# Performance work log

Hardware: AMD Instinct MI355X
Metric: run time of the kernel (lower is better)

## Reference

```python
import jax, jax.numpy as jnp
import numpy as np

K = 7  # kernel_size


def _patches(x, k):
    # x: [N, C, H, W] -> [K*K, N, C, H, W]; zero-padded local windows in
    # torch.nn.functional.unfold order (kernel positions row-major).
    N, C, H, W = x.shape
    p = k // 2
    xp = jnp.pad(x, ((0, 0), (0, 0), (p, p), (p, p)))
    return jnp.stack([xp[:, :, i:i + H, j:j + W]
                      for i in range(k) for j in range(k)], axis=0)


def setup_inputs() -> dict:
    key = jax.random.key(0)
    k1, k2 = jax.random.split(key)
    x = jax.random.normal(k1, (4, 128, 80, 80), dtype=jnp.float32)
    feat_in = jax.random.normal(k2, (4, 128, 80, 80), dtype=jnp.float32)
    return {"x": x, "feat_in": feat_in}


def reference(x, feat_in):
    N, C, H, W = feat_in.shape
    k2 = K * K
    # theta_x == phi_x == x in the original module.
    phi_p = _patches(x, K)                            # [K2, N, Cq, H, W]
    # local dot products: weight[k, n, h, w] = sum_c phi_window * theta_center
    w = jnp.einsum('knchw,nchw->knhw', phi_p, x)      # [K2, N, H, W]
    # L1-style normalization over the window (plain sum, as in the source)
    w = w / jnp.sum(w, axis=0, keepdims=True)
    feat_p = _patches(feat_in, K)                     # [K2, N, C, H, W]
    out = jnp.einsum('knhw,knchw->nchw', w, feat_p)   # [N, C, H, W]
    pairwise_weight = w.transpose(1, 2, 3, 0).reshape(N * H * W, 1, k2)
    return out, pairwise_weight
```

## Files before the change

### kernel.cpp

```cpp
#include <hip/hip_runtime.h>


namespace {

constexpr int CN = 4;
constexpr int CC = 128;
constexpr int HT = 80, WD = 80;
constexpr int KK = 7, K2 = 49, PD = 3;
constexpr int TW = 16, TH = 4;
constexpr int HW_ = TW + 6;
constexpr int HH_ = TH + 6;
constexpr int HENT = HW_ * HH_;
constexpr int HFLT = HENT * 4;
constexpr int HCHUNK = (HFLT + 63) / 64;
constexpr int HPADF = HCHUNK * 64;
constexpr int PLANE = HT * WD;
constexpr int GSTRIDE = 4 * PLANE;
constexpr int OUT_ELEMS = CN * CC * PLANE;

__device__ __forceinline__ void issue_chunks(const float* gbase, const int* off,
                                             float* lds, int tid) {
#if __has_builtin(__builtin_amdgcn_global_load_lds)
#pragma unroll
  for (int q = 0; q < HCHUNK; ++q) {
    __builtin_amdgcn_global_load_lds(
        (const __attribute__((address_space(1))) void*)(gbase + off[q]),
        (__attribute__((address_space(3))) void*)(lds + q * 64), 4, 0, 0);
  }
#else
#pragma unroll
  for (int q = 0; q < HCHUNK; ++q) lds[q * 64 + tid] = gbase[off[q]];
  asm volatile("s_waitcnt lgkmcnt(0)" ::: "memory");
#endif
}

#define WAIT_VM(n_lit)                                      \
  asm volatile("s_waitcnt vmcnt(" #n_lit ")" ::: "memory"); \
  __builtin_amdgcn_sched_barrier(0)

__global__ __launch_bounds__(64) void lnl2d_fused(const float* __restrict__ x,
                                                  const float* __restrict__ feat,
                                                  float* __restrict__ dout) {
  __shared__ float halo[2][HPADF];
  __shared__ float wstage[TH * TW * K2];

  const int tid = (int)threadIdx.x;
  const int tx = tid & (TW - 1);
  const int ty = tid >> 4;
  const int bx = (int)blockIdx.x;
  const int by = (int)blockIdx.y;
  const int n  = (int)blockIdx.z;

  const int h = by * TH + ty;
  const int w = bx * TW + tx;

  const float* xn = x + (size_t)n * CC * PLANE;
  const float* fn = feat + (size_t)n * CC * PLANE;
  float* out = dout;
  float* pw  = dout + OUT_ELEMS;

  int off[HCHUNK];
#pragma unroll
  for (int q = 0; q < HCHUNK; ++q) {
    int f = q * 64 + tid;
    int e = f >> 2;
    if (e > HENT - 1) e = HENT - 1;
    const int ch = f & 3;
    const int r  = e / HW_;
    const int cl = e - r * HW_;
    int gh = by * TH - PD + r;
    gh = gh < 0 ? 0 : (gh > HT - 1 ? HT - 1 : gh);
    int gw = bx * TW - PD + cl;
    gw = gw < 0 ? 0 : (gw > WD - 1 ? WD - 1 : gw);
    off[q] = ch * PLANE + gh * WD + gw;
  }

  float acc[K2];
#pragma unroll
  for (int k = 0; k < K2; ++k) acc[k] = 0.f;

  auto p1_compute = [&](const float* hb) {
    const float4 c4 = *(const float4*)(hb + ((ty + PD) * HW_ + (tx + PD)) * 4);
#pragma unroll
    for (int di = 0; di < KK; ++di) {
#pragma unroll
      for (int dj = 0; dj < KK; ++dj) {
        const float4 n4 = *(const float4*)(hb + ((ty + di) * HW_ + (tx + dj)) * 4);
        acc[di * KK + dj] += c4.x * n4.x + c4.y * n4.y + c4.z * n4.z + c4.w * n4.w;
      }
    }
  };

  issue_chunks(xn, off, halo[0], tid);
  int goff = GSTRIDE;
  for (int g = 0; g < 31; ++g) {
    issue_chunks(xn + goff, off, halo[(g + 1) & 1], tid);
    goff += GSTRIDE;
    WAIT_VM(14);
    p1_compute(halo[g & 1]);
  }
  issue_chunks(fn, off, halo[0], tid);
  WAIT_VM(14);
  p1_compute(halo[1]);

#pragma unroll
  for (int di = 0; di < KK; ++di) {
#pragma unroll
    for (int dj = 0; dj < KK; ++dj) {
      const int hh = h + di - PD, ww = w + dj - PD;
      if ((unsigned)hh >= (unsigned)HT || (unsigned)ww >= (unsigned)WD)
        acc[di * KK + dj] = 0.f;
    }
  }
  float ssum = 0.f;
#pragma unroll
  for (int k = 0; k < K2; ++k) ssum += acc[k];
  const float invs = 1.0f / ssum;
#pragma unroll
  for (int k = 0; k < K2; ++k) acc[k] *= invs;

#pragma unroll
  for (int k = 0; k < K2; ++k) wstage[tid * K2 + k] = acc[k];
  __syncthreads();
#pragma unroll
  for (int r = 0; r < TH; ++r) {
    float* dst = pw + (size_t)(n * PLANE + (by * TH + r) * WD + bx * TW) * K2;
    const float* src = wstage + r * TW * K2;
#pragma unroll
    for (int c2 = 0; c2 < (TW * K2) / 64; ++c2)
      dst[c2 * 64 + tid] = src[c2 * 64 + tid];
    if (tid < (TW * K2) - 64 * ((TW * K2) / 64))
      dst[64 * ((TW * K2) / 64) + tid] = src[64 * ((TW * K2) / 64) + tid];
  }

  const size_t obase = (size_t)n * CC * PLANE + (size_t)(h * WD + w);
  auto p2_compute = [&](const float* hb, int g) {
    float4 a = make_float4(0.f, 0.f, 0.f, 0.f);
#pragma unroll
    for (int di = 0; di < KK; ++di) {
#pragma unroll
      for (int dj = 0; dj < KK; ++dj) {
        const float4 n4 = *(const float4*)(hb + ((ty + di) * HW_ + (tx + dj)) * 4);
        const float wk = acc[di * KK + dj];
        a.x += wk * n4.x; a.y += wk * n4.y; a.z += wk * n4.z; a.w += wk * n4.w;
      }
    }
    out[obase + (size_t)(4 * g + 0) * PLANE] = a.x;
    out[obase + (size_t)(4 * g + 1) * PLANE] = a.y;
    out[obase + (size_t)(4 * g + 2) * PLANE] = a.z;
    out[obase + (size_t)(4 * g + 3) * PLANE] = a.w;
  };

  goff = GSTRIDE;
  for (int g = 0; g < 31; ++g) {
    issue_chunks(fn + goff, off, halo[(g + 1) & 1], tid);
    goff += GSTRIDE;
    WAIT_VM(14);
    p2_compute(halo[g & 1], g);
  }
  WAIT_VM(0);
  p2_compute(halo[1], 31);
}

}

extern "C" void kernel_launch(void* const* d_in, const int* in_sizes, int n_in,
                              void* d_out, int out_size, void* d_ws, size_t ws_size,
                              hipStream_t stream) {
  const float* x    = (const float*)d_in[0];
  const float* feat = (const float*)d_in[1];
  float* out        = (float*)d_out;
  dim3 grid(WD / TW, HT / TH, CN);
  lnl2d_fused<<<grid, 64, 0, stream>>>(x, feat, out);
}
```

Baseline: 170.1 us.

## Split fused kernel into channel-chunked correlation and aggregation kernels via workspace

```diff
diff --git a/kernel.cpp b/kernel.cpp
--- a/kernel.cpp
+++ b/kernel.cpp
@@ -3,63 +3,23 @@
 
 namespace {
 
-constexpr int CN = 4;
-constexpr int CC = 128;
-constexpr int HT = 80, WD = 80;
+constexpr int CN = 4, CC = 128, HT = 80, WD = 80;
 constexpr int KK = 7, K2 = 49, PD = 3;
 constexpr int TW = 16, TH = 4;
 constexpr int HW_ = TW + 6;
 constexpr int HH_ = TH + 6;
 constexpr int HENT = HW_ * HH_;
-constexpr int HFLT = HENT * 4;
-constexpr int HCHUNK = (HFLT + 63) / 64;
+constexpr int HCHUNK = (HENT * 4 + 63) / 64;
 constexpr int HPADF = HCHUNK * 64;
 constexpr int PLANE = HT * WD;
 constexpr int GSTRIDE = 4 * PLANE;
 constexpr int OUT_ELEMS = CN * CC * PLANE;
-
-__device__ __forceinline__ void issue_chunks(const float* gbase, const int* off,
-                                             float* lds, int tid) {
-#if __has_builtin(__builtin_amdgcn_global_load_lds)
-#pragma unroll
-  for (int q = 0; q < HCHUNK; ++q) {
-    __builtin_amdgcn_global_load_lds(
-        (const __attribute__((address_space(1))) void*)(gbase + off[q]),
-        (__attribute__((address_space(3))) void*)(lds + q * 64), 4, 0, 0);
-  }
-#else
-#pragma unroll
-  for (int q = 0; q < HCHUNK; ++q) lds[q * 64 + tid] = gbase[off[q]];
-  asm volatile("s_waitcnt lgkmcnt(0)" ::: "memory");
-#endif
-}
-
-#define WAIT_VM(n_lit)                                      \
-  asm volatile("s_waitcnt vmcnt(" #n_lit ")" ::: "memory"); \
-  __builtin_amdgcn_sched_barrier(0)
-
-__global__ __launch_bounds__(64) void lnl2d_fused(const float* __restrict__ x,
-                                                  const float* __restrict__ feat,
-                                                  float* __restrict__ dout) {
-  __shared__ float halo[2][HPADF];
-  __shared__ float wstage[TH * TW * K2];
-
-  const int tid = (int)threadIdx.x;
-  const int tx = tid & (TW - 1);
-  const int ty = tid >> 4;
-  const int bx = (int)blockIdx.x;
-  const int by = (int)blockIdx.y;
-  const int n  = (int)blockIdx.z;
-
-  const int h = by * TH + ty;
-  const int w = bx * TW + tx;
-
-  const float* xn = x + (size_t)n * CC * PLANE;
-  const float* fn = feat + (size_t)n * CC * PLANE;
-  float* out = dout;
-  float* pw  = dout + OUT_ELEMS;
-
-  int off[HCHUNK];
+constexpr int CHUNKS = 4, GPC = 8;
+constexpr int NTILES = 5 * 20 * CN;
+constexpr int WPAD = 52;
+constexpr size_t WS_NEED = (size_t)CHUNKS * NTILES * 64 * WPAD * 4;
+
+__device__ __forceinline__ void make_off(int* off, int bx, int by, int tid) {
 #pragma unroll
   for (int q = 0; q < HCHUNK; ++q) {
     int f = q * 64 + tid;
@@ -74,21 +34,218 @@
     gw = gw < 0 ? 0 : (gw > WD - 1 ? WD - 1 : gw);
     off[q] = ch * PLANE + gh * WD + gw;
   }
+}
+
+__device__ __forceinline__ void issue_chunks(const float* gbase, const int* off,
+                                             float* lds, int tid) {
+#if __has_builtin(__builtin_amdgcn_global_load_lds)
+#pragma unroll
+  for (int q = 0; q < HCHUNK; ++q) {
+    __builtin_amdgcn_global_load_lds(
+        (const __attribute__((address_space(1))) void*)(gbase + off[q]),
+        (__attribute__((address_space(3))) void*)(lds + q * 64), 4, 0, 0);
+  }
+#else
+#pragma unroll
+  for (int q = 0; q < HCHUNK; ++q) lds[q * 64 + tid] = gbase[off[q]];
+  asm volatile("s_waitcnt lgkmcnt(0)" ::: "memory");
+#endif
+}
+
+#define WAIT_VM(n_lit)                                      \
+  asm volatile("s_waitcnt vmcnt(" #n_lit ")" ::: "memory"); \
+  __builtin_amdgcn_sched_barrier(0)
+
+__global__ __launch_bounds__(64) void lnl2d_corr(const float* __restrict__ x,
+                                                 float* __restrict__ wpart) {
+  __shared__ float halo[3][HPADF];
+  __shared__ float wstage[64 * WPAD];
+
+  const int tid = (int)threadIdx.x;
+  const int tx = tid & (TW - 1), ty = tid >> 4;
+  const int bx = (int)blockIdx.x, by = (int)blockIdx.y;
+  const int z = (int)blockIdx.z, n = z >> 2, chunk = z & 3;
+  const int tile = (n * 20 + by) * 5 + bx;
+
+  const float* xc = x + (size_t)n * CC * PLANE + (size_t)chunk * 32 * PLANE;
+
+  int off[HCHUNK];
+  make_off(off, bx, by, tid);
 
   float acc[K2];
 #pragma unroll
   for (int k = 0; k < K2; ++k) acc[k] = 0.f;
 
-  auto p1_compute = [&](const float* hb) {
+  issue_chunks(xc, off, halo[0], tid);
+  issue_chunks(xc + GSTRIDE, off, halo[1], tid);
+  int goff = 2 * GSTRIDE;
+#pragma unroll
+  for (int g = 0; g < GPC; ++g) {
+    if (g < GPC - 2) { issue_chunks(xc + goff, off, halo[(g + 2) % 3], tid); goff += GSTRIDE; }
+    if (g < GPC - 2)      { WAIT_VM(28); }
+    else if (g == GPC - 2){ WAIT_VM(14); }
+    else                  { WAIT_VM(0); }
+    const float* hb = halo[g % 3];
     const float4 c4 = *(const float4*)(hb + ((ty + PD) * HW_ + (tx + PD)) * 4);
 #pragma unroll
-    for (int di = 0; di < KK; ++di) {
+    for (int di = 0; di < KK; ++di)
 #pragma unroll
       for (int dj = 0; dj < KK; ++dj) {
         const float4 n4 = *(const float4*)(hb + ((ty + di) * HW_ + (tx + dj)) * 4);
         acc[di * KK + dj] += c4.x * n4.x + c4.y * n4.y + c4.z * n4.z + c4.w * n4.w;
       }
+  }
+
+  const int h = by * TH + ty, w = bx * TW + tx;
+#pragma unroll
+  for (int di = 0; di < KK; ++di)
+#pragma unroll
+    for (int dj = 0; dj < KK; ++dj) {
+      const int hh = h + di - PD, ww = w + dj - PD;
+      if ((unsigned)hh >= (unsigned)HT || (unsigned)ww >= (unsigned)WD)
+        acc[di * KK + dj] = 0.f;
     }
+
+#pragma unroll
+  for (int k = 0; k < K2; ++k) wstage[tid * WPAD + k] = acc[k];
+#pragma unroll
+  for (int k = K2; k < WPAD; ++k) wstage[tid * WPAD + k] = 0.f;
+  __syncthreads();
+  float4* dst = (float4*)(wpart + ((size_t)(chunk * NTILES + tile) * 64) * WPAD);
+  const float4* src = (const float4*)wstage;
+#pragma unroll
+  for (int i = 0; i < (64 * WPAD) / 4 / 64; ++i)
+    dst[i * 64 + tid] = src[i * 64 + tid];
+}
+
+__global__ __launch_bounds__(64) void lnl2d_agg(const float* __restrict__ feat,
+                                                const float* __restrict__ wpart,
+                                                float* __restrict__ dout) {
+  __shared__ float halo[3][HPADF];
+  __shared__ float wstage[64 * WPAD];
+
+  const int tid = (int)threadIdx.x;
+  const int tx = tid & (TW - 1), ty = tid >> 4;
+  const int bx = (int)blockIdx.x, by = (int)blockIdx.y;
+  const int z = (int)blockIdx.z, n = z >> 2, chunk = z & 3;
+  const int tile = (n * 20 + by) * 5 + bx;
+  const int h = by * TH + ty, w = bx * TW + tx;
+
+  const float* fc = feat + (size_t)n * CC * PLANE + (size_t)chunk * 32 * PLANE;
+  float* out = dout;
+  float* pw  = dout + OUT_ELEMS;
+
+  int off[HCHUNK];
+  make_off(off, bx, by, tid);
+
+  float4 wv[WPAD / 4];
+#pragma unroll
+  for (int i = 0; i < WPAD / 4; ++i) wv[i] = make_float4(0.f, 0.f, 0.f, 0.f);
+#pragma unroll
+  for (int c = 0; c < CHUNKS; ++c) {
+    const float4* p =
+        (const float4*)(wpart + ((size_t)(c * NTILES + tile) * 64 + tid) * WPAD);
+#pragma unroll
+    for (int i = 0; i < WPAD / 4; ++i) {
+      const float4 v = p[i];
+      wv[i].x += v.x; wv[i].y += v.y; wv[i].z += v.z; wv[i].w += v.w;
+    }
+  }
+  float wk[K2];
+#pragma unroll
+  for (int k = 0; k < K2; ++k) wk[k] = ((const float*)wv)[k];
+  float ssum = 0.f;
+#pragma unroll
+  for (int k = 0; k < K2; ++k) ssum += wk[k];
+  const float invs = 1.0f / ssum;
+#pragma unroll
+  for (int k = 0; k < K2; ++k) wk[k] *= invs;
+
+  WAIT_VM(0);
+
+  float4 ov[GPC];
+#pragma unroll
+  for (int g = 0; g < GPC; ++g) ov[g] = make_float4(0.f, 0.f, 0.f, 0.f);
+
+  issue_chunks(fc, off, halo[0], tid);
+  issue_chunks(fc + GSTRIDE, off, halo[1], tid);
+  int goff = 2 * GSTRIDE;
+#pragma unroll
+  for (int g = 0; g < GPC; ++g) {
+    if (g < GPC - 2) { issue_chunks(fc + goff, off, halo[(g + 2) % 3], tid); goff += GSTRIDE; }
+    if (g < GPC - 2)      { WAIT_VM(28); }
+    else if (g == GPC - 2){ WAIT_VM(14); }
+    else                  { WAIT_VM(0); }
+    const float* hb = halo[g % 3];
+#pragma unroll
+    for (int di = 0; di < KK; ++di)
+#pragma unroll
+      for (int dj = 0; dj < KK; ++dj) {
+        const float4 n4 = *(const float4*)(hb + ((ty + di) * HW_ + (tx + dj)) * 4);
+        const float f = wk[di * KK + dj];
+        ov[g].x += f * n4.x; ov[g].y += f * n4.y; ov[g].z += f * n4.z; ov[g].w += f * n4.w;
+      }
+  }
+
+  const size_t ob = (size_t)n * CC * PLANE + (size_t)chunk * 32 * PLANE +
+                    (size_t)(h * WD + w);
+#pragma unroll
+  for (int g = 0; g < GPC; ++g) {
+    out[ob + (size_t)(4 * g + 0) * PLANE] = ov[g].x;
+    out[ob + (size_t)(4 * g + 1) * PLANE] = ov[g].y;
+    out[ob + (size_t)(4 * g + 2) * PLANE] = ov[g].z;
+    out[ob + (size_t)(4 * g + 3) * PLANE] = ov[g].w;
+  }
+
+  if (chunk == 0) {
+#pragma unroll
+    for (int k = 0; k < K2; ++k) wstage[tid * K2 + k] = wk[k];
+    __syncthreads();
+#pragma unroll
+    for (int r = 0; r < TH; ++r) {
+      float* dst = pw + (size_t)(n * PLANE + (by * TH + r) * WD + bx * TW) * K2;
+      const float* src = wstage + r * TW * K2;
+#pragma unroll
+      for (int c2 = 0; c2 < (TW * K2) / 64; ++c2)
+        dst[c2 * 64 + tid] = src[c2 * 64 + tid];
+      if (tid < (TW * K2) - 64 * ((TW * K2) / 64))
+        dst[64 * ((TW * K2) / 64) + tid] = src[64 * ((TW * K2) / 64) + tid];
+    }
+  }
+}
+
+__global__ __launch_bounds__(64) void lnl2d_fused(const float* __restrict__ x,
+                                                  const float* __restrict__ feat,
+                                                  float* __restrict__ dout) {
+  __shared__ float halo[2][HPADF];
+  __shared__ float wstage[TH * TW * K2];
+
+  const int tid = (int)threadIdx.x;
+  const int tx = tid & (TW - 1), ty = tid >> 4;
+  const int bx = (int)blockIdx.x, by = (int)blockIdx.y, n = (int)blockIdx.z;
+  const int h = by * TH + ty, w = bx * TW + tx;
+
+  const float* xn = x + (size_t)n * CC * PLANE;
+  const float* fn = feat + (size_t)n * CC * PLANE;
+  float* out = dout;
+  float* pw  = dout + OUT_ELEMS;
+
+  int off[HCHUNK];
+  make_off(off, bx, by, tid);
+
+  float acc[K2];
+#pragma unroll
+  for (int k = 0; k < K2; ++k) acc[k] = 0.f;
+
+  auto p1 = [&](const float* hb) {
+    const float4 c4 = *(const float4*)(hb + ((ty + PD) * HW_ + (tx + PD)) * 4);
+#pragma unroll
+    for (int di = 0; di < KK; ++di)
+#pragma unroll
+      for (int dj = 0; dj < KK; ++dj) {
+        const float4 n4 = *(const float4*)(hb + ((ty + di) * HW_ + (tx + dj)) * 4);
+        acc[di * KK + dj] += c4.x * n4.x + c4.y * n4.y + c4.z * n4.z + c4.w * n4.w;
+      }
   };
 
   issue_chunks(xn, off, halo[0], tid);
@@ -97,21 +254,20 @@
     issue_chunks(xn + goff, off, halo[(g + 1) & 1], tid);
     goff += GSTRIDE;
     WAIT_VM(14);
-    p1_compute(halo[g & 1]);
+    p1(halo[g & 1]);
   }
   issue_chunks(fn, off, halo[0], tid);
   WAIT_VM(14);
-  p1_compute(halo[1]);
-
-#pragma unroll
-  for (int di = 0; di < KK; ++di) {
+  p1(halo[1]);
+
+#pragma unroll
+  for (int di = 0; di < KK; ++di)
 #pragma unroll
     for (int dj = 0; dj < KK; ++dj) {
       const int hh = h + di - PD, ww = w + dj - PD;
       if ((unsigned)hh >= (unsigned)HT || (unsigned)ww >= (unsigned)WD)
         acc[di * KK + dj] = 0.f;
     }
-  }
   float ssum = 0.f;
 #pragma unroll
   for (int k = 0; k < K2; ++k) ssum += acc[k];
@@ -134,17 +290,16 @@
   }
 
   const size_t obase = (size_t)n * CC * PLANE + (size_t)(h * WD + w);
-  auto p2_compute = [&](const float* hb, int g) {
+  auto p2 = [&](const float* hb, int g) {
     float4 a = make_float4(0.f, 0.f, 0.f, 0.f);
 #pragma unroll
-    for (int di = 0; di < KK; ++di) {
+    for (int di = 0; di < KK; ++di)
 #pragma unroll
       for (int dj = 0; dj < KK; ++dj) {
         const float4 n4 = *(const float4*)(hb + ((ty + di) * HW_ + (tx + dj)) * 4);
-        const float wk = acc[di * KK + dj];
-        a.x += wk * n4.x; a.y += wk * n4.y; a.z += wk * n4.z; a.w += wk * n4.w;
+        const float f = acc[di * KK + dj];
+        a.x += f * n4.x; a.y += f * n4.y; a.z += f * n4.z; a.w += f * n4.w;
       }
-    }
     out[obase + (size_t)(4 * g + 0) * PLANE] = a.x;
     out[obase + (size_t)(4 * g + 1) * PLANE] = a.y;
     out[obase + (size_t)(4 * g + 2) * PLANE] = a.z;
@@ -156,10 +311,10 @@
     issue_chunks(fn + goff, off, halo[(g + 1) & 1], tid);
     goff += GSTRIDE;
     WAIT_VM(14);
-    p2_compute(halo[g & 1], g);
+    p2(halo[g & 1], g);
   }
   WAIT_VM(0);
-  p2_compute(halo[1], 31);
+  p2(halo[1], 31);
 }
 
 }
@@ -170,6 +325,14 @@
   const float* x    = (const float*)d_in[0];
   const float* feat = (const float*)d_in[1];
   float* out        = (float*)d_out;
-  dim3 grid(WD / TW, HT / TH, CN);
-  lnl2d_fused<<<grid, 64, 0, stream>>>(x, feat, out);
-}
+
+  if (ws_size >= WS_NEED) {
+    float* wpart = (float*)d_ws;
+    dim3 grid(5, 20, CN * CHUNKS);
+    lnl2d_corr<<<grid, 64, 0, stream>>>(x, wpart);
+    lnl2d_agg<<<grid, 64, 0, stream>>>(feat, wpart, out);
+  } else {
+    dim3 grid(5, 20, CN);
+    lnl2d_fused<<<grid, 64, 0, stream>>>(x, feat, out);
+  }
+}
```

Measured after the change: 142.9 us. -16.0%, faster.

## Split channel reduction across four waves per block with LDS atomic weight reduction

Applied to the files above, without the earlier changes.

```diff
diff --git a/kernel.cpp b/kernel.cpp
--- a/kernel.cpp
+++ b/kernel.cpp
@@ -3,66 +3,25 @@
 
 namespace {
 
-constexpr int CN = 4;
-constexpr int CC = 128;
-constexpr int HT = 80, WD = 80;
+constexpr int CN = 4, CC = 128, HT = 80, WD = 80;
 constexpr int KK = 7, K2 = 49, PD = 3;
 constexpr int TW = 16, TH = 4;
 constexpr int HW_ = TW + 6;
 constexpr int HH_ = TH + 6;
 constexpr int HENT = HW_ * HH_;
-constexpr int HFLT = HENT * 4;
-constexpr int HCHUNK = (HFLT + 63) / 64;
+constexpr int HCHUNK = (HENT * 4 + 63) / 64;
 constexpr int HPADF = HCHUNK * 64;
 constexpr int PLANE = HT * WD;
 constexpr int GSTRIDE = 4 * PLANE;
 constexpr int OUT_ELEMS = CN * CC * PLANE;
-
-__device__ __forceinline__ void issue_chunks(const float* gbase, const int* off,
-                                             float* lds, int tid) {
-#if __has_builtin(__builtin_amdgcn_global_load_lds)
+constexpr int NW = 4;
+constexpr int GPW = 8;
+constexpr int WR = 53;
+
+__device__ __forceinline__ void make_off(int* off, int bx, int by, int lane) {
 #pragma unroll
   for (int q = 0; q < HCHUNK; ++q) {
-    __builtin_amdgcn_global_load_lds(
-        (const __attribute__((address_space(1))) void*)(gbase + off[q]),
-        (__attribute__((address_space(3))) void*)(lds + q * 64), 4, 0, 0);
-  }
-#else
-#pragma unroll
-  for (int q = 0; q < HCHUNK; ++q) lds[q * 64 + tid] = gbase[off[q]];
-  asm volatile("s_waitcnt lgkmcnt(0)" ::: "memory");
-#endif
-}
-
-#define WAIT_VM(n_lit)                                      \
-  asm volatile("s_waitcnt vmcnt(" #n_lit ")" ::: "memory"); \
-  __builtin_amdgcn_sched_barrier(0)
-
-__global__ __launch_bounds__(64) void lnl2d_fused(const float* __restrict__ x,
-                                                  const float* __restrict__ feat,
-                                                  float* __restrict__ dout) {
-  __shared__ float halo[2][HPADF];
-  __shared__ float wstage[TH * TW * K2];
-
-  const int tid = (int)threadIdx.x;
-  const int tx = tid & (TW - 1);
-  const int ty = tid >> 4;
-  const int bx = (int)blockIdx.x;
-  const int by = (int)blockIdx.y;
-  const int n  = (int)blockIdx.z;
-
-  const int h = by * TH + ty;
-  const int w = bx * TW + tx;
-
-  const float* xn = x + (size_t)n * CC * PLANE;
-  const float* fn = feat + (size_t)n * CC * PLANE;
-  float* out = dout;
-  float* pw  = dout + OUT_ELEMS;
-
-  int off[HCHUNK];
-#pragma unroll
-  for (int q = 0; q < HCHUNK; ++q) {
-    int f = q * 64 + tid;
+    int f = q * 64 + lane;
     int e = f >> 2;
     if (e > HENT - 1) e = HENT - 1;
     const int ch = f & 3;
@@ -74,92 +33,169 @@
     gw = gw < 0 ? 0 : (gw > WD - 1 ? WD - 1 : gw);
     off[q] = ch * PLANE + gh * WD + gw;
   }
+}
+
+__device__ __forceinline__ void issue_chunks(const float* gbase, const int* off,
+                                             float* lds) {
+#if __has_builtin(__builtin_amdgcn_global_load_lds)
+#pragma unroll
+  for (int q = 0; q < HCHUNK; ++q) {
+    __builtin_amdgcn_global_load_lds(
+        (const __attribute__((address_space(1))) void*)(gbase + off[q]),
+        (__attribute__((address_space(3))) void*)(lds + q * 64), 4, 0, 0);
+  }
+#else
+  const int lane = (int)(threadIdx.x & 63);
+#pragma unroll
+  for (int q = 0; q < HCHUNK; ++q) lds[q * 64 + lane] = gbase[off[q]];
+  asm volatile("s_waitcnt lgkmcnt(0)" ::: "memory");
+#endif
+}
+
+#define WAIT_VM(n_lit)                                      \
+  asm volatile("s_waitcnt vmcnt(" #n_lit ")" ::: "memory"); \
+  __builtin_amdgcn_sched_barrier(0)
+
+__global__ __launch_bounds__(256) void lnl2d_fused4(
+    const float* __restrict__ x, const float* __restrict__ feat,
+    float* __restrict__ dout) {
+  __shared__ float halo[NW * 3][HPADF];
+  __shared__ float wred[64][WR];
+  __shared__ float inv[64];
+
+  const int tid  = (int)threadIdx.x;
+  const int wv   = tid >> 6;
+  const int lane = tid & 63;
+  const int tx = lane & (TW - 1), ty = lane >> 4;
+  const int bx = (int)blockIdx.x, by = (int)blockIdx.y, n = (int)blockIdx.z;
+  const int h = by * TH + ty, w = bx * TW + tx;
+
+  const float* xw = x + (size_t)n * CC * PLANE + (size_t)wv * 32 * PLANE;
+  const float* fw = feat + (size_t)n * CC * PLANE + (size_t)wv * 32 * PLANE;
+  float* out = dout;
+  float* pw  = dout + OUT_ELEMS;
+
+  int off[HCHUNK];
+  make_off(off, bx, by, lane);
+
+#pragma unroll
+  for (int i = 0; i < (64 * WR + 255) / 256; ++i) {
+    const int idx = i * 256 + tid;
+    if (idx < 64 * WR) ((float*)wred)[idx] = 0.f;
+  }
+  __syncthreads();
 
   float acc[K2];
 #pragma unroll
   for (int k = 0; k < K2; ++k) acc[k] = 0.f;
 
-  auto p1_compute = [&](const float* hb) {
+  float* hb0 = halo[wv * 3 + 0];
+  float* hb1 = halo[wv * 3 + 1];
+  float* hb2 = halo[wv * 3 + 2];
+
+  issue_chunks(xw, off, hb0);
+  issue_chunks(xw + GSTRIDE, off, hb1);
+  int goff = 2 * GSTRIDE;
+#pragma unroll
+  for (int g = 0; g < GPW; ++g) {
+    if (g < GPW - 2) {
+      float* dst = (g % 3 == 0) ? hb2 : ((g % 3 == 1) ? hb0 : hb1);
+      issue_chunks(xw + goff, off, dst);
+      goff += GSTRIDE;
+    }
+    if (g < GPW - 2)      { WAIT_VM(28); }
+    else if (g == GPW - 2){ WAIT_VM(14); }
+    else                  { WAIT_VM(0); }
+    const float* hb = (g % 3 == 0) ? hb0 : ((g % 3 == 1) ? hb1 : hb2);
     const float4 c4 = *(const float4*)(hb + ((ty + PD) * HW_ + (tx + PD)) * 4);
 #pragma unroll
-    for (int di = 0; di < KK; ++di) {
+    for (int di = 0; di < KK; ++di)
 #pragma unroll
       for (int dj = 0; dj < KK; ++dj) {
         const float4 n4 = *(const float4*)(hb + ((ty + di) * HW_ + (tx + dj)) * 4);
         acc[di * KK + dj] += c4.x * n4.x + c4.y * n4.y + c4.z * n4.z + c4.w * n4.w;
       }
-    }
-  };
-
-  issue_chunks(xn, off, halo[0], tid);
-  int goff = GSTRIDE;
-  for (int g = 0; g < 31; ++g) {
-    issue_chunks(xn + goff, off, halo[(g + 1) & 1], tid);
-    goff += GSTRIDE;
-    WAIT_VM(14);
-    p1_compute(halo[g & 1]);
-  }
-  issue_chunks(fn, off, halo[0], tid);
-  WAIT_VM(14);
-  p1_compute(halo[1]);
-
-#pragma unroll
-  for (int di = 0; di < KK; ++di) {
+  }
+
+#pragma unroll
+  for (int di = 0; di < KK; ++di)
 #pragma unroll
     for (int dj = 0; dj < KK; ++dj) {
       const int hh = h + di - PD, ww = w + dj - PD;
       if ((unsigned)hh >= (unsigned)HT || (unsigned)ww >= (unsigned)WD)
         acc[di * KK + dj] = 0.f;
     }
-  }
+#pragma unroll
+  for (int k = 0; k < K2; ++k) atomicAdd(&wred[lane][k], acc[k]);
+
+  __syncthreads();
+
+  issue_chunks(fw, off, hb0);
+  issue_chunks(fw + GSTRIDE, off, hb1);
+
+  float wk[K2];
   float ssum = 0.f;
 #pragma unroll
-  for (int k = 0; k < K2; ++k) ssum += acc[k];
+  for (int k = 0; k < K2; ++k) { wk[k] = wred[lane][k]; ssum += wk[k]; }
   const float invs = 1.0f / ssum;
 #pragma unroll
-  for (int k = 0; k < K2; ++k) acc[k] *= invs;
-
-#pragma unroll
-  for (int k = 0; k < K2; ++k) wstage[tid * K2 + k] = acc[k];
-  __syncthreads();
-#pragma unroll
-  for (int r = 0; r < TH; ++r) {
-    float* dst = pw + (size_t)(n * PLANE + (by * TH + r) * WD + bx * TW) * K2;
-    const float* src = wstage + r * TW * K2;
-#pragma unroll
-    for (int c2 = 0; c2 < (TW * K2) / 64; ++c2)
-      dst[c2 * 64 + tid] = src[c2 * 64 + tid];
-    if (tid < (TW * K2) - 64 * ((TW * K2) / 64))
-      dst[64 * ((TW * K2) / 64) + tid] = src[64 * ((TW * K2) / 64) + tid];
-  }
-
-  const size_t obase = (size_t)n * CC * PLANE + (size_t)(h * WD + w);
-  auto p2_compute = [&](const float* hb, int g) {
-    float4 a = make_float4(0.f, 0.f, 0.f, 0.f);
-#pragma unroll
-    for (int di = 0; di < KK; ++di) {
+  for (int k = 0; k < K2; ++k) wk[k] *= invs;
+  if (wv == 0) inv[lane] = invs;
+
+  float4 ov[GPW];
+#pragma unroll
+  for (int g = 0; g < GPW; ++g) ov[g] = make_float4(0.f, 0.f, 0.f, 0.f);
+
+  goff = 2 * GSTRIDE;
+#pragma unroll
+  for (int g = 0; g < GPW; ++g) {
+    if (g < GPW - 2) {
+      float* dst = (g % 3 == 0) ? hb2 : ((g % 3 == 1) ? hb0 : hb1);
+      issue_chunks(fw + goff, off, dst);
+      goff += GSTRIDE;
+    }
+    if (g < GPW - 2)      { WAIT_VM(28); }
+    else if (g == GPW - 2){ WAIT_VM(14); }
+    else                  { WAIT_VM(0); }
+    const float* hb = (g % 3 == 0) ? hb0 : ((g % 3 == 1) ? hb1 : hb2);
+#pragma unroll
+    for (int di = 0; di < KK; ++di)
 #pragma unroll
       for (int dj = 0; dj < KK; ++dj) {
         const float4 n4 = *(const float4*)(hb + ((ty + di) * HW_ + (tx + dj)) * 4);
-        const float wk = acc[di * KK + dj];
-        a.x += wk * n4.x; a.y += wk * n4.y; a.z += wk * n4.z; a.w += wk * n4.w;
+        const float f = wk[di * KK + dj];
+        ov[g].x += f * n4.x; ov[g].y += f * n4.y; ov[g].z += f * n4.z; ov[g].w += f * n4.w;
       }
-    }
-    out[obase + (size_t)(4 * g + 0) * PLANE] = a.x;
-    out[obase + (size_t)(4 * g + 1) * PLANE] = a.y;
-    out[obase + (size_t)(4 * g + 2) * PLANE] = a.z;
-    out[obase + (size_t)(4 * g + 3) * PLANE] = a.w;
-  };
-
-  goff = GSTRIDE;
-  for (int g = 0; g < 31; ++g) {
-    issue_chunks(fn + goff, off, halo[(g + 1) & 1], tid);
-    goff += GSTRIDE;
-    WAIT_VM(14);
-    p2_compute(halo[g & 1], g);
-  }
-  WAIT_VM(0);
-  p2_compute(halo[1], 31);
+  }
+
+  const size_t ob = (size_t)n * CC * PLANE + (size_t)wv * 32 * PLANE +
+                    (size_t)(h * WD + w);
+#pragma unroll
+  for (int g = 0; g < GPW; ++g) {
+    out[ob + (size_t)(4 * g + 0) * PLANE] = ov[g].x;
+    out[ob + (size_t)(4 * g + 1) * PLANE] = ov[g].y;
+    out[ob + (size_t)(4 * g + 2) * PLANE] = ov[g].z;
+    out[ob + (size_t)(4 * g + 3) * PLANE] = ov[g].w;
+  }
+
+  __syncthreads();
+
+#pragma unroll
+  for (int r = 0; r < TH; ++r) {
+    float* seg = pw + (size_t)(n * PLANE + (by * TH + r) * WD + bx * TW) * K2;
+#pragma unroll
+    for (int i = 0; i < (TW * K2) / 256; ++i) {
+      const int idx = i * 256 + tid;
+      const int col = idx / K2, k = idx - col * K2;
+      seg[idx] = wred[r * TW + col][k] * inv[r * TW + col];
+    }
+    const int rem = TW * K2 - 256 * ((TW * K2) / 256);
+    if (tid < rem) {
+      const int idx = 256 * ((TW * K2) / 256) + tid;
+      const int col = idx / K2, k = idx - col * K2;
+      seg[idx] = wred[r * TW + col][k] * inv[r * TW + col];
+    }
+  }
 }
 
 }
@@ -171,5 +207,5 @@
   const float* feat = (const float*)d_in[1];
   float* out        = (float*)d_out;
   dim3 grid(WD / TW, HT / TH, CN);
-  lnl2d_fused<<<grid, 64, 0, stream>>>(x, feat, out);
-}
+  lnl2d_fused4<<<grid, 256, 0, stream>>>(x, feat, out);
+}
```

New measurement: 137.9 us. 1.23x faster.
